# Kernel tuning notes

Hardware: AMD Instinct MI355X
Metric: run time of the kernel (lower is better)

## Reference

```python
import jax, jax.numpy as jnp
import numpy as np

B = 8
D_MODEL = 512
N_HEADS = 8
D_HEAD = 64
D_FF = 2048
N_ENC = 4
N_DEC = 4
SRC_LEN = 512
TGT_LEN = 512
PRED_LEN = 96
SRC_SIZE = 16
TGT_SIZE = 8
EPS = 1e-5
W_SCALE = 0.02


def setup_inputs() -> dict:
    key = jax.random.key(0)
    ks = iter(jax.random.split(key, 64))

    def w(shape):
        return jax.random.normal(next(ks), shape, dtype=jnp.float32) * W_SCALE

    d, f = D_MODEL, D_FF
    inp = {
        "src": jax.random.normal(next(ks), (B, SRC_LEN, SRC_SIZE), dtype=jnp.float32),
        "tgt": jax.random.normal(next(ks), (B, TGT_LEN, TGT_SIZE), dtype=jnp.float32),
        "src_pos_emb": w((SRC_LEN, d)),
        "tgt_pos_emb": w((TGT_LEN, d)),
        "src_lin_w": w((SRC_SIZE, d)), "src_lin_b": jnp.zeros((d,), jnp.float32),
        "tgt_lin_w": w((TGT_SIZE, d)), "tgt_lin_b": jnp.zeros((d,), jnp.float32),
        # encoder stacks [N_ENC, ...]
        "enc_wq": w((N_ENC, d, d)), "enc_wk": w((N_ENC, d, d)),
        "enc_wv": w((N_ENC, d, d)), "enc_wo": w((N_ENC, d, d)),
        "enc_ff1_w": w((N_ENC, d, f)), "enc_ff1_b": jnp.zeros((N_ENC, f), jnp.float32),
        "enc_ff2_w": w((N_ENC, f, d)), "enc_ff2_b": jnp.zeros((N_ENC, d), jnp.float32),
        "enc_ln1_g": jnp.ones((N_ENC, d), jnp.float32), "enc_ln1_b": jnp.zeros((N_ENC, d), jnp.float32),
        "enc_ln2_g": jnp.ones((N_ENC, d), jnp.float32), "enc_ln2_b": jnp.zeros((N_ENC, d), jnp.float32),
        # decoder stacks [N_DEC, ...]
        "dec_sa_wq": w((N_DEC, d, d)), "dec_sa_wk": w((N_DEC, d, d)),
        "dec_sa_wv": w((N_DEC, d, d)), "dec_sa_wo": w((N_DEC, d, d)),
        "dec_ca_wq": w((N_DEC, d, d)), "dec_ca_wk": w((N_DEC, d, d)),
        "dec_ca_wv": w((N_DEC, d, d)), "dec_ca_wo": w((N_DEC, d, d)),
        "dec_ff1_w": w((N_DEC, d, f)), "dec_ff1_b": jnp.zeros((N_DEC, f), jnp.float32),
        "dec_ff2_w": w((N_DEC, f, d)), "dec_ff2_b": jnp.zeros((N_DEC, d), jnp.float32),
        "dec_ln1_g": jnp.ones((N_DEC, d), jnp.float32), "dec_ln1_b": jnp.zeros((N_DEC, d), jnp.float32),
        "dec_ln2_g": jnp.ones((N_DEC, d), jnp.float32), "dec_ln2_b": jnp.zeros((N_DEC, d), jnp.float32),
        "dec_ln3_g": jnp.ones((N_DEC, d), jnp.float32), "dec_ln3_b": jnp.zeros((N_DEC, d), jnp.float32),
        "proj_w": w((d, TGT_SIZE)), "proj_b": jnp.zeros((TGT_SIZE,), jnp.float32),
    }
    return inp


def layer_norm(x, g, b):
    mu = jnp.mean(x, axis=-1, keepdims=True)
    var = jnp.mean(jnp.square(x - mu), axis=-1, keepdims=True)
    return (x - mu) * jax.lax.rsqrt(var + EPS) * g + b


def mha(x_q, x_kv, wq, wk, wv, wo, mask):
    Bq, Lq, _ = x_q.shape
    Lk = x_kv.shape[1]
    q = (x_q @ wq).reshape(Bq, Lq, N_HEADS, D_HEAD)
    k = (x_kv @ wk).reshape(Bq, Lk, N_HEADS, D_HEAD)
    v = (x_kv @ wv).reshape(Bq, Lk, N_HEADS, D_HEAD)
    scores = jnp.einsum("bqhd,bkhd->bhqk", q, k) / jnp.sqrt(
        jnp.asarray(D_HEAD, jnp.float32))
    if mask is not None:
        scores = scores + mask  # broadcast over batch/heads
    attn = jax.nn.softmax(scores, axis=-1)
    ctx = jnp.einsum("bhqk,bkhd->bqhd", attn, v).reshape(Bq, Lq, N_HEADS * D_HEAD)
    return ctx @ wo


def dec_self_mask():
    # get_subsequence_mask with pt=0: -inf on last PRED_LEN key columns
    m = jnp.zeros((TGT_LEN, TGT_LEN), jnp.float32)
    return m.at[:, -PRED_LEN:].set(-jnp.inf)


def reference(src, tgt, src_pos_emb, tgt_pos_emb, src_lin_w, src_lin_b,
              tgt_lin_w, tgt_lin_b,
              enc_wq, enc_wk, enc_wv, enc_wo, enc_ff1_w, enc_ff1_b,
              enc_ff2_w, enc_ff2_b, enc_ln1_g, enc_ln1_b, enc_ln2_g, enc_ln2_b,
              dec_sa_wq, dec_sa_wk, dec_sa_wv, dec_sa_wo,
              dec_ca_wq, dec_ca_wk, dec_ca_wv, dec_ca_wo,
              dec_ff1_w, dec_ff1_b, dec_ff2_w, dec_ff2_b,
              dec_ln1_g, dec_ln1_b, dec_ln2_g, dec_ln2_b, dec_ln3_g, dec_ln3_b,
              proj_w, proj_b):
    # input projections + positional embedding (dropout disabled, eval mode)
    enc_x = src_pos_emb[None] + src @ src_lin_w + src_lin_b
    dec_x = tgt_pos_emb[None] + tgt @ tgt_lin_w + tgt_lin_b

    # encoder (enc_self_attn_mask is None)
    for i in range(N_ENC):
        a = mha(enc_x, enc_x, enc_wq[i], enc_wk[i], enc_wv[i], enc_wo[i], None)
        enc_x = layer_norm(a + enc_x, enc_ln1_g[i], enc_ln1_b[i])
        h = jax.nn.relu(enc_x @ enc_ff1_w[i] + enc_ff1_b[i]) @ enc_ff2_w[i] + enc_ff2_b[i]
        enc_x = layer_norm(h + enc_x, enc_ln2_g[i], enc_ln2_b[i])

    sa_mask = dec_self_mask()  # [tgt_len, tgt_len]
    for i in range(N_DEC):
        a = mha(dec_x, dec_x, dec_sa_wq[i], dec_sa_wk[i], dec_sa_wv[i],
                dec_sa_wo[i], sa_mask)
        dec_x = layer_norm(a + dec_x, dec_ln1_g[i], dec_ln1_b[i])
        a = mha(dec_x, enc_x, dec_ca_wq[i], dec_ca_wk[i], dec_ca_wv[i],
                dec_ca_wo[i], None)
        dec_x = layer_norm(a + dec_x, dec_ln2_g[i], dec_ln2_b[i])
        h = jax.nn.relu(dec_x @ dec_ff1_w[i] + dec_ff1_b[i]) @ dec_ff2_w[i] + dec_ff2_b[i]
        dec_x = layer_norm(h + dec_x, dec_ln3_g[i], dec_ln3_b[i])

    return dec_x @ proj_w + proj_b  # [B, tgt_len, tgt_size]
```

## Files before the change

### kernel.cpp

```cpp
#include <hip/hip_runtime.h>
#include <hip/hip_bf16.h>
#include <math.h>

#define D_MODEL 512
#define N_HEADS 8
#define D_HEAD  64
#define D_FF    2048
#define SEQ     512
#define BATCH   8
#define ROWS    (BATCH * SEQ)
#define PRED_LEN 96
#define KLEN_MASKED (SEQ - PRED_LEN)
#define LN_EPS  1e-5f

typedef float  f32x4 __attribute__((ext_vector_type(4)));
typedef short  s16x8 __attribute__((ext_vector_type(8)));

__device__ __forceinline__ float bf2f(ushort u) {
    union { unsigned int i; float f; } c; c.i = ((unsigned int)u) << 16; return c.f;
}
__device__ __forceinline__ ushort f2bf(float v) {
    __hip_bfloat16 h = __float2bfloat16(v);
    return *(ushort*)&h;
}
__device__ __forceinline__ void gl_lds16(const void* g, void* lds) {
    __builtin_amdgcn_global_load_lds(
        (const __attribute__((address_space(1))) unsigned int*)g,
        (__attribute__((address_space(3))) unsigned int*)lds, 16, 0, 0);
}

__device__ __forceinline__ void swz8(int& x, int& y, int gx, int gy) {
    int n = gx * gy;
    int id = x + gx * y;
    int id2 = (id & 7) * (n >> 3) + (id >> 3);
    x = id2 % gx;
    y = id2 / gx;
}

struct GDesc {
    const ushort* A; int lda;
    const ushort* Bt; int ldb;
    ushort* C; int ldc;
    int N; int K;
    const float* bias; int relu;
    ushort* VT; int vcol0;
};

__device__ __forceinline__ void gemm_body(const GDesc& d, int bx, int by)
{
    __shared__ __attribute__((aligned(16))) ushort As[2][128 * 64];
    __shared__ __attribute__((aligned(16))) ushort Bs[2][64 * 64];
    const int tid = threadIdx.x;
    const int w = tid >> 6, lane = tid & 63;
    const int l16 = lane & 15, quad = lane >> 4;
    const int m0 = by * 128, n0 = bx * 64;
    const ushort* Ab = d.A + (size_t)m0 * d.lda;
    const ushort* Bb = d.Bt + (size_t)n0 * d.ldb;
    const int wm = (w >> 1) * 64, wn = (w & 1) * 32;
    const int nk = d.K >> 6;
    const int lr = lane >> 3, lc = lane & 7;
    const int ch = lc ^ lr;

    auto stage = [&](int buf, int k0) {
        #pragma unroll
        for (int q = 0; q < 4; ++q) {
            int seg = q * 4 + w;
            int row = seg * 8 + lr;
            gl_lds16(Ab + (size_t)row * d.lda + k0 + ch * 8,
                     (void*)(As[buf] + seg * 512));
        }
        #pragma unroll
        for (int q = 0; q < 2; ++q) {
            int seg = q * 4 + w;
            int row = seg * 8 + lr;
            gl_lds16(Bb + (size_t)row * d.ldb + k0 + ch * 8,
                     (void*)(Bs[buf] + seg * 512));
        }
    };

    f32x4 acc[4][2];
    #pragma unroll
    for (int i = 0; i < 4; ++i)
        #pragma unroll
        for (int j = 0; j < 2; ++j) acc[i][j] = (f32x4)0.f;

    auto compute = [&](int buf) {
        #pragma unroll
        for (int t2 = 0; t2 < 2; ++t2) {
            s16x8 af[4];
            #pragma unroll
            for (int i = 0; i < 4; ++i) {
                int r = wm + i * 16 + l16;
                int p = (t2 * 4 + quad) ^ (r & 7);
                af[i] = *(const s16x8*)(As[buf] + r * 64 + p * 8);
            }
            #pragma unroll
            for (int j = 0; j < 2; ++j) {
                int r = wn + j * 16 + l16;
                int p = (t2 * 4 + quad) ^ (r & 7);
                s16x8 bfr = *(const s16x8*)(Bs[buf] + r * 64 + p * 8);
                #pragma unroll
                for (int i = 0; i < 4; ++i)
                    acc[i][j] = __builtin_amdgcn_mfma_f32_16x16x32_bf16(af[i], bfr, acc[i][j], 0, 0, 0);
            }
        }
    };

    stage(0, 0);
    __syncthreads();
    int cur = 0;
    for (int t = 0; t < nk - 1; ++t) {
        stage(cur ^ 1, (t + 1) << 6);
        compute(cur);
        __syncthreads();
        cur ^= 1;
    }
    compute(cur);

    const bool isv = (d.VT != nullptr) && (n0 >= d.vcol0);
    if (isv) {
        #pragma unroll
        for (int i = 0; i < 4; ++i) {
            int mrow = m0 + wm + i * 16 + quad * 4;
            int b = mrow >> 9, pbase = mrow & 511;
            #pragma unroll
            for (int j = 0; j < 2; ++j) {
                int cv = n0 + wn + j * 16 + l16 - d.vcol0;
                int h = cv >> 6, dd = cv & 63;
                union { ushort u[4]; uint2 v; } pk;
                #pragma unroll
                for (int r = 0; r < 4; ++r) pk.u[r] = f2bf(acc[i][j][r]);
                *(uint2*)(d.VT + ((size_t)((b * 8 + h) * 64 + dd) * 512 + pbase)) = pk.v;
            }
        }
    } else {
        #pragma unroll
        for (int i = 0; i < 4; ++i) {
            #pragma unroll
            for (int j = 0; j < 2; ++j) {
                int col = n0 + wn + j * 16 + l16;
                float bv = d.bias ? d.bias[col] : 0.f;
                #pragma unroll
                for (int r = 0; r < 4; ++r) {
                    float v = acc[i][j][r] + bv;
                    if (d.relu) v = fmaxf(v, 0.f);
                    d.C[(size_t)(m0 + wm + i * 16 + quad * 4 + r) * d.ldc + col] = f2bf(v);
                }
            }
        }
    }
}

__global__ __launch_bounds__(256) void gemm_one(GDesc d)
{
    int bx = blockIdx.x, by = blockIdx.y;
    swz8(bx, by, gridDim.x, gridDim.y);
    if (bx * 64 < d.N) gemm_body(d, bx, by);
}

__global__ __launch_bounds__(256) void gemm_two(GDesc d0, GDesc d1)
{
    const GDesc& d = blockIdx.z ? d1 : d0;
    int bx = blockIdx.x, by = blockIdx.y;
    swz8(bx, by, gridDim.x, gridDim.y);
    if (bx * 64 < d.N) gemm_body(d, bx, by);
}

struct SKDesc {
    const ushort* A; int lda;
    const ushort* Bt; int ldb;
    float* P;
    int K;
};

__global__ __launch_bounds__(256) void gemm_sk(SKDesc d)
{
    __shared__ __attribute__((aligned(16))) ushort As[2][128 * 64];
    __shared__ __attribute__((aligned(16))) ushort Bs[2][64 * 64];
    const int tid = threadIdx.x;
    const int w = tid >> 6, lane = tid & 63;
    const int l16 = lane & 15, quad = lane >> 4;
    int bx = blockIdx.x, by = blockIdx.y;
    swz8(bx, by, gridDim.x, gridDim.y);
    const int m0 = by * 128, n0 = bx * 64;
    const int slice = blockIdx.z;
    const int kb = slice * (d.K >> 1);
    const int nk = d.K >> 7;
    const ushort* Ab = d.A + (size_t)m0 * d.lda + kb;
    const ushort* Bb = d.Bt + (size_t)n0 * d.ldb + kb;
    const int wm = (w >> 1) * 64, wn = (w & 1) * 32;
    const int lr = lane >> 3, lc = lane & 7;
    const int ch = lc ^ lr;

    auto stage = [&](int buf, int k0) {
        #pragma unroll
        for (int q = 0; q < 4; ++q) {
            int seg = q * 4 + w;
            int row = seg * 8 + lr;
            gl_lds16(Ab + (size_t)row * d.lda + k0 + ch * 8,
                     (void*)(As[buf] + seg * 512));
        }
        #pragma unroll
        for (int q = 0; q < 2; ++q) {
            int seg = q * 4 + w;
            int row = seg * 8 + lr;
            gl_lds16(Bb + (size_t)row * d.ldb + k0 + ch * 8,
                     (void*)(Bs[buf] + seg * 512));
        }
    };

    f32x4 acc[4][2];
    #pragma unroll
    for (int i = 0; i < 4; ++i)
        #pragma unroll
        for (int j = 0; j < 2; ++j) acc[i][j] = (f32x4)0.f;

    auto compute = [&](int buf) {
        #pragma unroll
        for (int t2 = 0; t2 < 2; ++t2) {
            s16x8 af[4];
            #pragma unroll
            for (int i = 0; i < 4; ++i) {
                int r = wm + i * 16 + l16;
                int p = (t2 * 4 + quad) ^ (r & 7);
                af[i] = *(const s16x8*)(As[buf] + r * 64 + p * 8);
            }
            #pragma unroll
            for (int j = 0; j < 2; ++j) {
                int r = wn + j * 16 + l16;
                int p = (t2 * 4 + quad) ^ (r & 7);
                s16x8 bfr = *(const s16x8*)(Bs[buf] + r * 64 + p * 8);
                #pragma unroll
                for (int i = 0; i < 4; ++i)
                    acc[i][j] = __builtin_amdgcn_mfma_f32_16x16x32_bf16(af[i], bfr, acc[i][j], 0, 0, 0);
            }
        }
    };

    stage(0, 0);
    __syncthreads();
    int cur = 0;
    for (int t = 0; t < nk - 1; ++t) {
        stage(cur ^ 1, (t + 1) << 6);
        compute(cur);
        __syncthreads();
        cur ^= 1;
    }
    compute(cur);

    float* P = d.P + (size_t)slice * ((size_t)ROWS * 512);
    #pragma unroll
    for (int i = 0; i < 4; ++i) {
        #pragma unroll
        for (int j = 0; j < 2; ++j) {
            int col = n0 + wn + j * 16 + l16;
            #pragma unroll
            for (int r = 0; r < 4; ++r)
                P[(size_t)(m0 + wm + i * 16 + quad * 4 + r) * 512 + col] = acc[i][j][r];
        }
    }
}

__global__ __launch_bounds__(256) void flash_attn(
    const ushort* __restrict__ Q, int ldq,
    const ushort* __restrict__ K, int ldk,
    const ushort* __restrict__ Vt,
    ushort* __restrict__ O, int ldo, int klen)
{
    __shared__ __attribute__((aligned(16))) ushort KVs[8192];
    __shared__ __attribute__((aligned(16))) ushort Es[4][2048];
    const int tid = threadIdx.x, w = tid >> 6, lane = tid & 63;
    const int l16 = lane & 15, quad = lane >> 4;
    int bqx = blockIdx.x, bhy = blockIdx.y;
    swz8(bqx, bhy, gridDim.x, gridDim.y);
    const int bh = bhy, b = bh >> 3, h = bh & 7;
    const int q0 = bqx * 64;

    const ushort* Qb = Q + (size_t)(b * SEQ) * ldq + h * D_HEAD;
    const ushort* Kb = K + (size_t)(b * SEQ) * ldk + h * D_HEAD;
    const ushort* Vb = Vt + (size_t)bh * (D_HEAD * SEQ);

    auto stageK = [&](int kc) {
        #pragma unroll
        for (int it = 0; it < 4; ++it) {
            int cc = (it * 4 + w) * 64 + lane;
            int row = cc >> 3;
            int dch = (cc & 7) ^ (row & 7);
            gl_lds16(Kb + (size_t)(kc * 128 + row) * ldk + dch * 8,
                     (void*)(KVs + (size_t)(it * 4 + w) * 512));
        }
    };
    auto stageV = [&](int kc) {
        #pragma unroll
        for (int it = 0; it < 4; ++it) {
            int cc = (it * 4 + w) * 64 + lane;
            int dd = cc >> 4;
            int kch = (cc & 15) ^ (dd & 15);
            gl_lds16(Vb + (size_t)dd * SEQ + kc * 128 + kch * 8,
                     (void*)(KVs + (size_t)(it * 4 + w) * 512));
        }
    };

    stageK(0);

    s16x8 af0, af1;
    {
        const ushort* qr = Qb + (size_t)(q0 + w * 16 + l16) * ldq + quad * 8;
        af0 = *(const s16x8*)(qr);
        af1 = *(const s16x8*)(qr + 32);
    }

    f32x4 sc[32];

    #pragma unroll
    for (int kc = 0; kc < 4; ++kc) {
        if (kc > 0) stageK(kc);
        __syncthreads();
        #pragma unroll
        for (int kt = 0; kt < 8; ++kt) {
            int r0 = kt * 16 + l16;
            s16x8 b0 = *(const s16x8*)(KVs + r0 * 64 + ((quad)     ^ (r0 & 7)) * 8);
            s16x8 b1 = *(const s16x8*)(KVs + r0 * 64 + ((4 + quad) ^ (r0 & 7)) * 8);
            f32x4 a = __builtin_amdgcn_mfma_f32_16x16x32_bf16(af0, b0, (f32x4)0.f, 0, 0, 0);
            sc[kc * 8 + kt] = __builtin_amdgcn_mfma_f32_16x16x32_bf16(af1, b1, a, 0, 0, 0);
        }
        __syncthreads();
    }

    stageV(0);

    float inv[4];
    #pragma unroll
    for (int r = 0; r < 4; ++r) {
        float m = -1e30f;
        #pragma unroll
        for (int j = 0; j < 32; ++j) {
            bool valid = (j * 16 + l16) < klen;
            m = valid ? fmaxf(m, sc[j][r]) : m;
        }
        m = fmaxf(m, __shfl_xor(m, 1));
        m = fmaxf(m, __shfl_xor(m, 2));
        m = fmaxf(m, __shfl_xor(m, 4));
        m = fmaxf(m, __shfl_xor(m, 8));
        float ssum = 0.f;
        #pragma unroll
        for (int j = 0; j < 32; ++j) {
            bool valid = (j * 16 + l16) < klen;
            float e = valid ? __expf((sc[j][r] - m) * 0.125f) : 0.f;
            sc[j][r] = e;
            ssum += e;
        }
        ssum += __shfl_xor(ssum, 1);
        ssum += __shfl_xor(ssum, 2);
        ssum += __shfl_xor(ssum, 4);
        ssum += __shfl_xor(ssum, 8);
        inv[r] = 1.f / ssum;
    }

    f32x4 oacc[4];
    #pragma unroll
    for (int jd = 0; jd < 4; ++jd) oacc[jd] = (f32x4)0.f;
    #pragma unroll
    for (int kc = 0; kc < 4; ++kc) {
        if (kc > 0) stageV(kc);
        #pragma unroll
        for (int j = 0; j < 8; ++j) {
            int lcj = j * 2 + (l16 >> 3);
            #pragma unroll
            for (int r = 0; r < 4; ++r) {
                int m = quad * 4 + r;
                Es[w][m * 128 + (lcj ^ m) * 8 + (l16 & 7)] = f2bf(sc[kc * 8 + j][r]);
            }
        }
        __syncthreads();
        #pragma unroll
        for (int ks = 0; ks < 4; ++ks) {
            int lc = ks * 4 + quad;
            s16x8 ea = *(const s16x8*)(&Es[w][l16 * 128 + (lc ^ l16) * 8]);
            #pragma unroll
            for (int jd = 0; jd < 4; ++jd) {
                int row = jd * 16 + l16;
                s16x8 vb = *(const s16x8*)(KVs + row * 128 + (lc ^ l16) * 8);
                oacc[jd] = __builtin_amdgcn_mfma_f32_16x16x32_bf16(ea, vb, oacc[jd], 0, 0, 0);
            }
        }
        __syncthreads();
    }

    ushort* Ob = O + (size_t)(b * SEQ) * ldo + h * D_HEAD;
    #pragma unroll
    for (int jd = 0; jd < 4; ++jd)
        #pragma unroll
        for (int r = 0; r < 4; ++r)
            Ob[(size_t)(q0 + w * 16 + quad * 4 + r) * ldo + jd * 16 + l16] =
                f2bf(oacc[jd][r] * inv[r]);
}

struct AttnPtrs { const float* p[48]; };
struct FfPtrs   { const float* p[16]; };

__global__ __launch_bounds__(256) void repack_attn(AttnPtrs L, ushort* __restrict__ out)
{
    int z = blockIdx.z;
    const float* in = L.p[z];
    ushort* o = out + (size_t)z * 262144;
    __shared__ float t[32][33];
    int n0 = blockIdx.x * 32, k0 = blockIdx.y * 32;
    int tx = threadIdx.x & 31, ty = threadIdx.x >> 5;
    #pragma unroll
    for (int r = 0; r < 4; ++r)
        t[ty + r * 8][tx] = in[(size_t)(k0 + ty + r * 8) * 512 + n0 + tx];
    __syncthreads();
    #pragma unroll
    for (int r = 0; r < 4; ++r)
        o[(size_t)(n0 + ty + r * 8) * 512 + k0 + tx] = f2bf(t[tx][ty + r * 8]);
}

__global__ __launch_bounds__(256) void repack_ff(FfPtrs L, ushort* __restrict__ out)
{
    int z = blockIdx.y;
    int Kd = (z < 8) ? 512 : 2048, Nd = (z < 8) ? 2048 : 512;
    const float* in = L.p[z];
    ushort* o = out + (size_t)z * (512 * 2048);
    int t = blockIdx.x;
    int tn = Nd / 32;
    int n0 = (t % tn) * 32, k0 = (t / tn) * 32;
    __shared__ float ts[32][33];
    int tx = threadIdx.x & 31, ty = threadIdx.x >> 5;
    #pragma unroll
    for (int r = 0; r < 4; ++r)
        ts[ty + r * 8][tx] = in[(size_t)(k0 + ty + r * 8) * Nd + n0 + tx];
    __syncthreads();
    #pragma unroll
    for (int r = 0; r < 4; ++r)
        o[(size_t)(n0 + ty + r * 8) * Kd + k0 + tx] = f2bf(ts[tx][ty + r * 8]);
}

__global__ __launch_bounds__(256) void input_proj2(
    const float* __restrict__ x0, const float* __restrict__ w0,
    const float* __restrict__ b0, const float* __restrict__ p0,
    float* __restrict__ o0_32, ushort* __restrict__ o0_b, int in0,
    const float* __restrict__ x1, const float* __restrict__ w1,
    const float* __restrict__ b1, const float* __restrict__ p1,
    float* __restrict__ o1_32, ushort* __restrict__ o1_b, int in1)
{
    const int z = blockIdx.y;
    const float* x = z ? x1 : x0;  const float* w = z ? w1 : w0;
    const float* bias = z ? b1 : b0; const float* pos = z ? p1 : p0;
    float* out32 = z ? o1_32 : o0_32; ushort* outb = z ? o1_b : o0_b;
    int in_size = z ? in1 : in0;
    int idx = blockIdx.x * 256 + threadIdx.x;
    int col = idx & (D_MODEL - 1);
    int row = idx >> 9;
    int l   = row & (SEQ - 1);
    const float* xr = x + (size_t)row * in_size;
    float acc = bias[col] + pos[(size_t)l * D_MODEL + col];
    for (int t = 0; t < in_size; ++t) acc += xr[t] * w[(size_t)t * D_MODEL + col];
    out32[idx] = acc;
    outb[idx]  = f2bf(acc);
}

__global__ __launch_bounds__(256) void add_ln2(
    const float* __restrict__ p, const float* __restrict__ gb,
    const float* __restrict__ x,
    const float* __restrict__ g, const float* __restrict__ b,
    float* __restrict__ out32, ushort* __restrict__ outb)
{
    const int row  = blockIdx.x * 4 + (threadIdx.x >> 6);
    const int lane = threadIdx.x & 63;
    const int c0   = lane * 8;
    const size_t base = (size_t)row * D_MODEL + c0;
    const float* p1 = p + (size_t)ROWS * 512;
    f32x4 a0 = *(const f32x4*)(p + base),  a1 = *(const f32x4*)(p + base + 4);
    f32x4 c0v= *(const f32x4*)(p1 + base), c1v= *(const f32x4*)(p1 + base + 4);
    f32x4 x0 = *(const f32x4*)(x + base),  x1 = *(const f32x4*)(x + base + 4);
    float v[8];
    #pragma unroll
    for (int j = 0; j < 4; ++j) {
        v[j]     = a0[j] + c0v[j] + x0[j];
        v[4 + j] = a1[j] + c1v[j] + x1[j];
    }
    if (gb) {
        f32x4 gb0 = *(const f32x4*)(gb + c0), gb1 = *(const f32x4*)(gb + c0 + 4);
        #pragma unroll
        for (int j = 0; j < 4; ++j) { v[j] += gb0[j]; v[4 + j] += gb1[j]; }
    }
    float s = 0.f;
    #pragma unroll
    for (int j = 0; j < 8; ++j) s += v[j];
    #pragma unroll
    for (int off = 32; off; off >>= 1) s += __shfl_xor(s, off);
    float mu = s * (1.f / D_MODEL);
    float q = 0.f;
    #pragma unroll
    for (int j = 0; j < 8; ++j) { v[j] -= mu; q += v[j] * v[j]; }
    #pragma unroll
    for (int off = 32; off; off >>= 1) q += __shfl_xor(q, off);
    float rs = rsqrtf(q * (1.f / D_MODEL) + LN_EPS);
    f32x4 g0 = *(const f32x4*)(g + c0), g1 = *(const f32x4*)(g + c0 + 4);
    f32x4 b0 = *(const f32x4*)(b + c0), b1 = *(const f32x4*)(b + c0 + 4);
    f32x4 y0, y1;
    union { ushort u[8]; s16x8 w; } pk;
    #pragma unroll
    for (int j = 0; j < 4; ++j) {
        y0[j] = v[j]     * rs * g0[j] + b0[j];
        y1[j] = v[4 + j] * rs * g1[j] + b1[j];
        pk.u[j]     = f2bf(y0[j]);
        pk.u[4 + j] = f2bf(y1[j]);
    }
    *(f32x4*)(out32 + base)     = y0;
    *(f32x4*)(out32 + base + 4) = y1;
    *(s16x8*)(outb + base)      = pk.w;
}

__global__ __launch_bounds__(256) void final_proj(
    const float* __restrict__ X, const float* __restrict__ W,
    const float* __restrict__ b, float* __restrict__ out)
{
    const int row  = blockIdx.x * 4 + (threadIdx.x >> 6);
    const int lane = threadIdx.x & 63;
    const float* xr = X + (size_t)row * D_MODEL + lane * 8;
    f32x4 x0 = *(const f32x4*)(xr), x1 = *(const f32x4*)(xr + 4);
    const float* wr = W + (size_t)lane * 64;
    f32x4 pa = (f32x4)0.f, pb = (f32x4)0.f;
    #pragma unroll
    for (int j = 0; j < 8; ++j) {
        float xv = (j < 4) ? x0[j] : x1[j - 4];
        f32x4 w0 = *(const f32x4*)(wr + j * 8);
        f32x4 w1 = *(const f32x4*)(wr + j * 8 + 4);
        #pragma unroll
        for (int c = 0; c < 4; ++c) { pa[c] += xv * w0[c]; pb[c] += xv * w1[c]; }
    }
    #pragma unroll
    for (int off = 32; off; off >>= 1) {
        #pragma unroll
        for (int c = 0; c < 4; ++c) {
            pa[c] += __shfl_xor(pa[c], off);
            pb[c] += __shfl_xor(pb[c], off);
        }
    }
    if (lane == 0) {
        float* o = out + (size_t)row * 8;
        #pragma unroll
        for (int c = 0; c < 4; ++c) { o[c] = pa[c] + b[c]; o[4 + c] = pb[c] + b[4 + c]; }
    }
}

extern "C" void kernel_launch(void* const* d_in, const int* in_sizes, int n_in,
                              void* d_out, int out_size, void* d_ws, size_t ws_size,
                              hipStream_t stream)
{
    const float* src         = (const float*)d_in[0];
    const float* tgt         = (const float*)d_in[1];
    const float* src_pos     = (const float*)d_in[2];
    const float* tgt_pos     = (const float*)d_in[3];
    const float* src_lin_w   = (const float*)d_in[4];
    const float* src_lin_b   = (const float*)d_in[5];
    const float* tgt_lin_w   = (const float*)d_in[6];
    const float* tgt_lin_b   = (const float*)d_in[7];
    const float* enc_wq      = (const float*)d_in[8];
    const float* enc_wk      = (const float*)d_in[9];
    const float* enc_wv      = (const float*)d_in[10];
    const float* enc_wo      = (const float*)d_in[11];
    const float* enc_ff1_w   = (const float*)d_in[12];
    const float* enc_ff1_b   = (const float*)d_in[13];
    const float* enc_ff2_w   = (const float*)d_in[14];
    const float* enc_ff2_b   = (const float*)d_in[15];
    const float* enc_ln1_g   = (const float*)d_in[16];
    const float* enc_ln1_b   = (const float*)d_in[17];
    const float* enc_ln2_g   = (const float*)d_in[18];
    const float* enc_ln2_b   = (const float*)d_in[19];
    const float* dec_sa_wq   = (const float*)d_in[20];
    const float* dec_sa_wk   = (const float*)d_in[21];
    const float* dec_sa_wv   = (const float*)d_in[22];
    const float* dec_sa_wo   = (const float*)d_in[23];
    const float* dec_ca_wq   = (const float*)d_in[24];
    const float* dec_ca_wk   = (const float*)d_in[25];
    const float* dec_ca_wv   = (const float*)d_in[26];
    const float* dec_ca_wo   = (const float*)d_in[27];
    const float* dec_ff1_w   = (const float*)d_in[28];
    const float* dec_ff1_b   = (const float*)d_in[29];
    const float* dec_ff2_w   = (const float*)d_in[30];
    const float* dec_ff2_b   = (const float*)d_in[31];
    const float* dec_ln1_g   = (const float*)d_in[32];
    const float* dec_ln1_b   = (const float*)d_in[33];
    const float* dec_ln2_g   = (const float*)d_in[34];
    const float* dec_ln2_b   = (const float*)d_in[35];
    const float* dec_ln3_g   = (const float*)d_in[36];
    const float* dec_ln3_b   = (const float*)d_in[37];
    const float* proj_w      = (const float*)d_in[38];
    const float* proj_b      = (const float*)d_in[39];

    char* p = (char*)d_ws;
    auto carve = [&](size_t bytes) { char* r = p; p += (bytes + 255) & ~(size_t)255; return r; };
    ushort* enc_xb = (ushort*)carve((size_t)ROWS * D_MODEL * 2);
    ushort* dec_xb = (ushort*)carve((size_t)ROWS * D_MODEL * 2);
    float*  enc_x32= (float*) carve((size_t)ROWS * D_MODEL * 4);
    float*  dec_x32= (float*) carve((size_t)ROWS * D_MODEL * 4);
    ushort* qkvb   = (ushort*)carve((size_t)ROWS * 1536 * 2);
    ushort* qb     = (ushort*)carve((size_t)ROWS * D_MODEL * 2);
    ushort* kvb    = (ushort*)carve((size_t)ROWS * 1024 * 2);
    ushort* ctxb   = (ushort*)carve((size_t)ROWS * D_MODEL * 2);
    float*  pf     = (float*) carve((size_t)2 * ROWS * D_MODEL * 4);
    ushort* ffhb   = (ushort*)carve((size_t)ROWS * D_FF * 2);
    ushort* vt     = (ushort*)carve((size_t)64 * D_HEAD * SEQ * 2);
    ushort* wa     = (ushort*)carve((size_t)48 * 262144 * 2);
    ushort* wf     = (ushort*)carve((size_t)16 * 1048576 * 2);

    const dim3 blk(256);

    {
        AttnPtrs A;
        for (int i = 0; i < 4; ++i) {
            const size_t o = (size_t)i * 262144;
            A.p[i * 3 + 0] = enc_wq + o;  A.p[i * 3 + 1] = enc_wk + o;  A.p[i * 3 + 2] = enc_wv + o;
            A.p[12 + i] = enc_wo + o;
            A.p[16 + i * 3 + 0] = dec_sa_wq + o; A.p[16 + i * 3 + 1] = dec_sa_wk + o;
            A.p[16 + i * 3 + 2] = dec_sa_wv + o;
            A.p[28 + i] = dec_sa_wo + o;
            A.p[32 + i * 2 + 0] = dec_ca_wk + o; A.p[32 + i * 2 + 1] = dec_ca_wv + o;
            A.p[40 + i] = dec_ca_wq + o;
            A.p[44 + i] = dec_ca_wo + o;
        }
        repack_attn<<<dim3(16, 16, 48), blk, 0, stream>>>(A, wa);
        FfPtrs F;
        for (int i = 0; i < 4; ++i) {
            F.p[0 + i]  = enc_ff1_w + (size_t)i * 1048576;
            F.p[4 + i]  = dec_ff1_w + (size_t)i * 1048576;
            F.p[8 + i]  = enc_ff2_w + (size_t)i * 1048576;
            F.p[12 + i] = dec_ff2_w + (size_t)i * 1048576;
        }
        repack_ff<<<dim3(1024, 16), blk, 0, stream>>>(F, wf);
    }

    auto mkd = [&](const ushort* A, int lda, const ushort* Bt, int ldb,
                   ushort* C, int ldc, int N, int K,
                   const float* bias, int relu, ushort* VT, int vcol0) {
        GDesc d; d.A = A; d.lda = lda; d.Bt = Bt; d.ldb = ldb;
        d.C = C; d.ldc = ldc; d.N = N; d.K = K;
        d.bias = bias; d.relu = relu; d.VT = VT; d.vcol0 = vcol0;
        return d;
    };
    auto g64 = [&](const GDesc& d) {
        gemm_one<<<dim3(d.N / 64, ROWS / 128), blk, 0, stream>>>(d);
    };
    auto gsk = [&](const ushort* A, int lda, const ushort* Bt, int K) {
        SKDesc d; d.A = A; d.lda = lda; d.Bt = Bt; d.ldb = K; d.P = pf; d.K = K;
        gemm_sk<<<dim3(8, ROWS / 128, 2), blk, 0, stream>>>(d);
    };

    input_proj2<<<dim3(ROWS * D_MODEL / 256, 2), blk, 0, stream>>>(
        src, src_lin_w, src_lin_b, src_pos, enc_x32, enc_xb, 16,
        tgt, tgt_lin_w, tgt_lin_b, tgt_pos, dec_x32, dec_xb, 8);

    for (int i = 0; i < 4; ++i) {
        g64(mkd(enc_xb, 512, wa + (size_t)(i * 3) * 262144, 512, qkvb, 1536,
                1536, 512, nullptr, 0, vt, 1024));
        flash_attn<<<dim3(8, 64), blk, 0, stream>>>(qkvb, 1536, qkvb + 512, 1536, vt,
                                                    ctxb, D_MODEL, SEQ);
        gsk(ctxb, 512, wa + (size_t)(12 + i) * 262144, 512);
        add_ln2<<<ROWS / 4, blk, 0, stream>>>(pf, nullptr, enc_x32,
                                              enc_ln1_g + i * 512, enc_ln1_b + i * 512,
                                              enc_x32, enc_xb);
        g64(mkd(enc_xb, 512, wf + (size_t)i * 1048576, 512, ffhb, 2048,
                2048, 512, enc_ff1_b + i * 2048, 1, nullptr, 0));
        gsk(ffhb, 2048, wf + (size_t)(8 + i) * 1048576, 2048);
        add_ln2<<<ROWS / 4, blk, 0, stream>>>(pf, enc_ff2_b + i * 512, enc_x32,
                                              enc_ln2_g + i * 512, enc_ln2_b + i * 512,
                                              enc_x32, enc_xb);
    }

    for (int i = 0; i < 4; ++i) {
        g64(mkd(dec_xb, 512, wa + (size_t)(16 + i * 3) * 262144, 512, qkvb, 1536,
                1536, 512, nullptr, 0, vt, 1024));
        flash_attn<<<dim3(8, 64), blk, 0, stream>>>(qkvb, 1536, qkvb + 512, 1536, vt,
                                                    ctxb, D_MODEL, KLEN_MASKED);
        gsk(ctxb, 512, wa + (size_t)(28 + i) * 262144, 512);
        add_ln2<<<ROWS / 4, blk, 0, stream>>>(pf, nullptr, dec_x32,
                                              dec_ln1_g + i * 512, dec_ln1_b + i * 512,
                                              dec_x32, dec_xb);
        {
            GDesc dq = mkd(dec_xb, 512, wa + (size_t)(40 + i) * 262144, 512, qb, 512,
                           512, 512, nullptr, 0, nullptr, 0);
            GDesc dkv = mkd(enc_xb, 512, wa + (size_t)(32 + i * 2) * 262144, 512, kvb, 1024,
                            1024, 512, nullptr, 0, vt, 512);
            gemm_two<<<dim3(16, ROWS / 128, 2), blk, 0, stream>>>(dq, dkv);
        }
        flash_attn<<<dim3(8, 64), blk, 0, stream>>>(qb, 512, kvb, 1024, vt,
                                                    ctxb, D_MODEL, SEQ);
        gsk(ctxb, 512, wa + (size_t)(44 + i) * 262144, 512);
        add_ln2<<<ROWS / 4, blk, 0, stream>>>(pf, nullptr, dec_x32,
                                              dec_ln2_g + i * 512, dec_ln2_b + i * 512,
                                              dec_x32, dec_xb);
        g64(mkd(dec_xb, 512, wf + (size_t)(4 + i) * 1048576, 512, ffhb, 2048,
                2048, 512, dec_ff1_b + i * 2048, 1, nullptr, 0));
        gsk(ffhb, 2048, wf + (size_t)(12 + i) * 1048576, 2048);
        add_ln2<<<ROWS / 4, blk, 0, stream>>>(pf, dec_ff2_b + i * 512, dec_x32,
                                              dec_ln3_g + i * 512, dec_ln3_b + i * 512,
                                              dec_x32, dec_xb);
    }

    final_proj<<<ROWS / 4, blk, 0, stream>>>(dec_x32, proj_w, proj_b, (float*)d_out);
}
```

Before: 1.228 ms.

## Batch encoder and decoder layer-0 self-attention blocks into shared launches

The decoder's first self-attention block does not depend on the encoder, so its QKV GEMM, flash attention, output-projection split-K GEMM and add+LayerNorm are now launched together with the encoder's layer-0 equivalents. Each pair runs as one kernel selected by grid z or y. This halves the launch count for those stages and fills the GPU with twice as many blocks. It needs duplicate scratch buffers (qkvb2, vt2, ctxb2, pf2) and adds a descriptor select in each kernel.

Result: no change. 1.248 ms (+1.6%).

```diff
diff --git a/kernel.cpp b/kernel.cpp
--- a/kernel.cpp
+++ b/kernel.cpp
@@ -173,7 +173,7 @@
     int K;
 };
 
-__global__ __launch_bounds__(256) void gemm_sk(SKDesc d)
+__device__ __forceinline__ void sk_body(const SKDesc& d, int slice)
 {
     __shared__ __attribute__((aligned(16))) ushort As[2][128 * 64];
     __shared__ __attribute__((aligned(16))) ushort Bs[2][64 * 64];
@@ -183,7 +183,6 @@
     int bx = blockIdx.x, by = blockIdx.y;
     swz8(bx, by, gridDim.x, gridDim.y);
     const int m0 = by * 128, n0 = bx * 64;
-    const int slice = blockIdx.z;
     const int kb = slice * (d.K >> 1);
     const int nk = d.K >> 7;
     const ushort* Ab = d.A + (size_t)m0 * d.lda + kb;
@@ -261,11 +260,24 @@
     }
 }
 
-__global__ __launch_bounds__(256) void flash_attn(
-    const ushort* __restrict__ Q, int ldq,
-    const ushort* __restrict__ K, int ldk,
-    const ushort* __restrict__ Vt,
-    ushort* __restrict__ O, int ldo, int klen)
+__global__ __launch_bounds__(256) void gemm_sk(SKDesc d)
+{
+    sk_body(d, blockIdx.z);
+}
+
+__global__ __launch_bounds__(256) void gemm_sk2(SKDesc d0, SKDesc d1)
+{
+    sk_body((blockIdx.z >> 1) ? d1 : d0, blockIdx.z & 1);
+}
+
+struct FA {
+    const ushort* Q; int ldq;
+    const ushort* K; int ldk;
+    const ushort* Vt;
+    ushort* O; int ldo; int klen;
+};
+
+__device__ __forceinline__ void flash_body(const FA& f)
 {
     __shared__ __attribute__((aligned(16))) ushort KVs[8192];
     __shared__ __attribute__((aligned(16))) ushort Es[4][2048];
@@ -276,9 +288,9 @@
     const int bh = bhy, b = bh >> 3, h = bh & 7;
     const int q0 = bqx * 64;
 
-    const ushort* Qb = Q + (size_t)(b * SEQ) * ldq + h * D_HEAD;
-    const ushort* Kb = K + (size_t)(b * SEQ) * ldk + h * D_HEAD;
-    const ushort* Vb = Vt + (size_t)bh * (D_HEAD * SEQ);
+    const ushort* Qb = f.Q + (size_t)(b * SEQ) * f.ldq + h * D_HEAD;
+    const ushort* Kb = f.K + (size_t)(b * SEQ) * f.ldk + h * D_HEAD;
+    const ushort* Vb = f.Vt + (size_t)bh * (D_HEAD * SEQ);
 
     auto stageK = [&](int kc) {
         #pragma unroll
@@ -286,7 +298,7 @@
             int cc = (it * 4 + w) * 64 + lane;
             int row = cc >> 3;
             int dch = (cc & 7) ^ (row & 7);
-            gl_lds16(Kb + (size_t)(kc * 128 + row) * ldk + dch * 8,
+            gl_lds16(Kb + (size_t)(kc * 128 + row) * f.ldk + dch * 8,
                      (void*)(KVs + (size_t)(it * 4 + w) * 512));
         }
     };
@@ -305,7 +317,7 @@
 
     s16x8 af0, af1;
     {
-        const ushort* qr = Qb + (size_t)(q0 + w * 16 + l16) * ldq + quad * 8;
+        const ushort* qr = Qb + (size_t)(q0 + w * 16 + l16) * f.ldq + quad * 8;
         af0 = *(const s16x8*)(qr);
         af1 = *(const s16x8*)(qr + 32);
     }
@@ -335,7 +347,7 @@
         float m = -1e30f;
         #pragma unroll
         for (int j = 0; j < 32; ++j) {
-            bool valid = (j * 16 + l16) < klen;
+            bool valid = (j * 16 + l16) < f.klen;
             m = valid ? fmaxf(m, sc[j][r]) : m;
         }
         m = fmaxf(m, __shfl_xor(m, 1));
@@ -345,7 +357,7 @@
         float ssum = 0.f;
         #pragma unroll
         for (int j = 0; j < 32; ++j) {
-            bool valid = (j * 16 + l16) < klen;
+            bool valid = (j * 16 + l16) < f.klen;
             float e = valid ? __expf((sc[j][r] - m) * 0.125f) : 0.f;
             sc[j][r] = e;
             ssum += e;
@@ -387,13 +399,20 @@
         __syncthreads();
     }
 
-    ushort* Ob = O + (size_t)(b * SEQ) * ldo + h * D_HEAD;
+    ushort* Ob = f.O + (size_t)(b * SEQ) * f.ldo + h * D_HEAD;
     #pragma unroll
     for (int jd = 0; jd < 4; ++jd)
         #pragma unroll
         for (int r = 0; r < 4; ++r)
-            Ob[(size_t)(q0 + w * 16 + quad * 4 + r) * ldo + jd * 16 + l16] =
+            Ob[(size_t)(q0 + w * 16 + quad * 4 + r) * f.ldo + jd * 16 + l16] =
                 f2bf(oacc[jd][r] * inv[r]);
+}
+
+__global__ __launch_bounds__(256) void flash_one(FA f) { flash_body(f); }
+
+__global__ __launch_bounds__(256) void flash_two(FA f0, FA f1)
+{
+    flash_body(blockIdx.z ? f1 : f0);
 }
 
 struct AttnPtrs { const float* p[48]; };
@@ -460,28 +479,31 @@
     outb[idx]  = f2bf(acc);
 }
 
-__global__ __launch_bounds__(256) void add_ln2(
-    const float* __restrict__ p, const float* __restrict__ gb,
-    const float* __restrict__ x,
-    const float* __restrict__ g, const float* __restrict__ b,
-    float* __restrict__ out32, ushort* __restrict__ outb)
+struct LN {
+    const float* p; const float* gb;
+    const float* x;
+    const float* g; const float* b;
+    float* out32; ushort* outb;
+};
+
+__device__ __forceinline__ void ln_body(const LN& d)
 {
     const int row  = blockIdx.x * 4 + (threadIdx.x >> 6);
     const int lane = threadIdx.x & 63;
     const int c0   = lane * 8;
     const size_t base = (size_t)row * D_MODEL + c0;
-    const float* p1 = p + (size_t)ROWS * 512;
-    f32x4 a0 = *(const f32x4*)(p + base),  a1 = *(const f32x4*)(p + base + 4);
-    f32x4 c0v= *(const f32x4*)(p1 + base), c1v= *(const f32x4*)(p1 + base + 4);
-    f32x4 x0 = *(const f32x4*)(x + base),  x1 = *(const f32x4*)(x + base + 4);
+    const float* p1 = d.p + (size_t)ROWS * 512;
+    f32x4 a0 = *(const f32x4*)(d.p + base),  a1 = *(const f32x4*)(d.p + base + 4);
+    f32x4 c0v= *(const f32x4*)(p1 + base),   c1v= *(const f32x4*)(p1 + base + 4);
+    f32x4 x0 = *(const f32x4*)(d.x + base),  x1 = *(const f32x4*)(d.x + base + 4);
     float v[8];
     #pragma unroll
     for (int j = 0; j < 4; ++j) {
         v[j]     = a0[j] + c0v[j] + x0[j];
         v[4 + j] = a1[j] + c1v[j] + x1[j];
     }
-    if (gb) {
-        f32x4 gb0 = *(const f32x4*)(gb + c0), gb1 = *(const f32x4*)(gb + c0 + 4);
+    if (d.gb) {
+        f32x4 gb0 = *(const f32x4*)(d.gb + c0), gb1 = *(const f32x4*)(d.gb + c0 + 4);
         #pragma unroll
         for (int j = 0; j < 4; ++j) { v[j] += gb0[j]; v[4 + j] += gb1[j]; }
     }
@@ -497,8 +519,8 @@
     #pragma unroll
     for (int off = 32; off; off >>= 1) q += __shfl_xor(q, off);
     float rs = rsqrtf(q * (1.f / D_MODEL) + LN_EPS);
-    f32x4 g0 = *(const f32x4*)(g + c0), g1 = *(const f32x4*)(g + c0 + 4);
-    f32x4 b0 = *(const f32x4*)(b + c0), b1 = *(const f32x4*)(b + c0 + 4);
+    f32x4 g0 = *(const f32x4*)(d.g + c0), g1 = *(const f32x4*)(d.g + c0 + 4);
+    f32x4 b0 = *(const f32x4*)(d.b + c0), b1 = *(const f32x4*)(d.b + c0 + 4);
     f32x4 y0, y1;
     union { ushort u[8]; s16x8 w; } pk;
     #pragma unroll
@@ -508,9 +530,16 @@
         pk.u[j]     = f2bf(y0[j]);
         pk.u[4 + j] = f2bf(y1[j]);
     }
-    *(f32x4*)(out32 + base)     = y0;
-    *(f32x4*)(out32 + base + 4) = y1;
-    *(s16x8*)(outb + base)      = pk.w;
+    *(f32x4*)(d.out32 + base)     = y0;
+    *(f32x4*)(d.out32 + base + 4) = y1;
+    *(s16x8*)(d.outb + base)      = pk.w;
+}
+
+__global__ __launch_bounds__(256) void add_ln_one(LN d) { ln_body(d); }
+
+__global__ __launch_bounds__(256) void add_ln_two(LN d0, LN d1)
+{
+    ln_body(blockIdx.y ? d1 : d0);
 }
 
 __global__ __launch_bounds__(256) void final_proj(
@@ -598,12 +627,16 @@
     float*  enc_x32= (float*) carve((size_t)ROWS * D_MODEL * 4);
     float*  dec_x32= (float*) carve((size_t)ROWS * D_MODEL * 4);
     ushort* qkvb   = (ushort*)carve((size_t)ROWS * 1536 * 2);
+    ushort* qkvb2  = (ushort*)carve((size_t)ROWS * 1536 * 2);
     ushort* qb     = (ushort*)carve((size_t)ROWS * D_MODEL * 2);
     ushort* kvb    = (ushort*)carve((size_t)ROWS * 1024 * 2);
     ushort* ctxb   = (ushort*)carve((size_t)ROWS * D_MODEL * 2);
+    ushort* ctxb2  = (ushort*)carve((size_t)ROWS * D_MODEL * 2);
     float*  pf     = (float*) carve((size_t)2 * ROWS * D_MODEL * 4);
+    float*  pf2    = (float*) carve((size_t)2 * ROWS * D_MODEL * 4);
     ushort* ffhb   = (ushort*)carve((size_t)ROWS * D_FF * 2);
     ushort* vt     = (ushort*)carve((size_t)64 * D_HEAD * SEQ * 2);
+    ushort* vt2    = (ushort*)carve((size_t)64 * D_HEAD * SEQ * 2);
     ushort* wa     = (ushort*)carve((size_t)48 * 262144 * 2);
     ushort* wf     = (ushort*)carve((size_t)16 * 1048576 * 2);
 
@@ -641,44 +674,81 @@
         d.bias = bias; d.relu = relu; d.VT = VT; d.vcol0 = vcol0;
         return d;
     };
+    auto mksk = [&](const ushort* A, int lda, const ushort* Bt, int K, float* P) {
+        SKDesc d; d.A = A; d.lda = lda; d.Bt = Bt; d.ldb = K; d.P = P; d.K = K;
+        return d;
+    };
+    auto mkfa = [&](const ushort* Q, int ldq, const ushort* K, int ldk,
+                    const ushort* Vt, ushort* O, int klen) {
+        FA f; f.Q = Q; f.ldq = ldq; f.K = K; f.ldk = ldk; f.Vt = Vt;
+        f.O = O; f.ldo = D_MODEL; f.klen = klen;
+        return f;
+    };
+    auto mkln = [&](const float* pp, const float* gb, float* x32,
+                    const float* g, const float* b, ushort* outb) {
+        LN d; d.p = pp; d.gb = gb; d.x = x32; d.g = g; d.b = b;
+        d.out32 = x32; d.outb = outb;
+        return d;
+    };
     auto g64 = [&](const GDesc& d) {
         gemm_one<<<dim3(d.N / 64, ROWS / 128), blk, 0, stream>>>(d);
-    };
-    auto gsk = [&](const ushort* A, int lda, const ushort* Bt, int K) {
-        SKDesc d; d.A = A; d.lda = lda; d.Bt = Bt; d.ldb = K; d.P = pf; d.K = K;
-        gemm_sk<<<dim3(8, ROWS / 128, 2), blk, 0, stream>>>(d);
     };
 
     input_proj2<<<dim3(ROWS * D_MODEL / 256, 2), blk, 0, stream>>>(
         src, src_lin_w, src_lin_b, src_pos, enc_x32, enc_xb, 16,
         tgt, tgt_lin_w, tgt_lin_b, tgt_pos, dec_x32, dec_xb, 8);
 
+    {
+        GDesc qe = mkd(enc_xb, 512, wa, 512, qkvb, 1536, 1536, 512,
+                       nullptr, 0, vt, 1024);
+        GDesc qd = mkd(dec_xb, 512, wa + (size_t)16 * 262144, 512, qkvb2, 1536,
+                       1536, 512, nullptr, 0, vt2, 1024);
+        gemm_two<<<dim3(24, ROWS / 128, 2), blk, 0, stream>>>(qe, qd);
+
+        FA fe = mkfa(qkvb, 1536, qkvb + 512, 1536, vt, ctxb, SEQ);
+        FA fd = mkfa(qkvb2, 1536, qkvb2 + 512, 1536, vt2, ctxb2, KLEN_MASKED);
+        flash_two<<<dim3(8, 64, 2), blk, 0, stream>>>(fe, fd);
+
+        SKDesc se = mksk(ctxb, 512, wa + (size_t)12 * 262144, 512, pf);
+        SKDesc sd = mksk(ctxb2, 512, wa + (size_t)28 * 262144, 512, pf2);
+        gemm_sk2<<<dim3(8, ROWS / 128, 4), blk, 0, stream>>>(se, sd);
+
+        LN le = mkln(pf, nullptr, enc_x32, enc_ln1_g, enc_ln1_b, enc_xb);
+        LN ld = mkln(pf2, nullptr, dec_x32, dec_ln1_g, dec_ln1_b, dec_xb);
+        add_ln_two<<<dim3(ROWS / 4, 2), blk, 0, stream>>>(le, ld);
+    }
+
     for (int i = 0; i < 4; ++i) {
-        g64(mkd(enc_xb, 512, wa + (size_t)(i * 3) * 262144, 512, qkvb, 1536,
-                1536, 512, nullptr, 0, vt, 1024));
-        flash_attn<<<dim3(8, 64), blk, 0, stream>>>(qkvb, 1536, qkvb + 512, 1536, vt,
-                                                    ctxb, D_MODEL, SEQ);
-        gsk(ctxb, 512, wa + (size_t)(12 + i) * 262144, 512);
-        add_ln2<<<ROWS / 4, blk, 0, stream>>>(pf, nullptr, enc_x32,
-                                              enc_ln1_g + i * 512, enc_ln1_b + i * 512,
-                                              enc_x32, enc_xb);
+        if (i > 0) {
+            g64(mkd(enc_xb, 512, wa + (size_t)(i * 3) * 262144, 512, qkvb, 1536,
+                    1536, 512, nullptr, 0, vt, 1024));
+            flash_one<<<dim3(8, 64), blk, 0, stream>>>(
+                mkfa(qkvb, 1536, qkvb + 512, 1536, vt, ctxb, SEQ));
+            gemm_sk<<<dim3(8, ROWS / 128, 2), blk, 0, stream>>>(
+                mksk(ctxb, 512, wa + (size_t)(12 + i) * 262144, 512, pf));
+            add_ln_one<<<ROWS / 4, blk, 0, stream>>>(
+                mkln(pf, nullptr, enc_x32, enc_ln1_g + i * 512, enc_ln1_b + i * 512, enc_xb));
+        }
         g64(mkd(enc_xb, 512, wf + (size_t)i * 1048576, 512, ffhb, 2048,
                 2048, 512, enc_ff1_b + i * 2048, 1, nullptr, 0));
-        gsk(ffhb, 2048, wf + (size_t)(8 + i) * 1048576, 2048);
-        add_ln2<<<ROWS / 4, blk, 0, stream>>>(pf, enc_ff2_b + i * 512, enc_x32,
-                                              enc_ln2_g + i * 512, enc_ln2_b + i * 512,
-                                              enc_x32, enc_xb);
+        gemm_sk<<<dim3(8, ROWS / 128, 2), blk, 0, stream>>>(
+            mksk(ffhb, 2048, wf + (size_t)(8 + i) * 1048576, 2048, pf));
+        add_ln_one<<<ROWS / 4, blk, 0, stream>>>(
+            mkln(pf, enc_ff2_b + i * 512, enc_x32,
+                 enc_ln2_g + i * 512, enc_ln2_b + i * 512, enc_xb));
     }
 
     for (int i = 0; i < 4; ++i) {
-        g64(mkd(dec_xb, 512, wa + (size_t)(16 + i * 3) * 262144, 512, qkvb, 1536,
-                1536, 512, nullptr, 0, vt, 1024));
-        flash_attn<<<dim3(8, 64), blk, 0, stream>>>(qkvb, 1536, qkvb + 512, 1536, vt,
-                                                    ctxb, D_MODEL, KLEN_MASKED);
-        gsk(ctxb, 512, wa + (size_t)(28 + i) * 262144, 512);
-        add_ln2<<<ROWS / 4, blk, 0, stream>>>(pf, nullptr, dec_x32,
-                                              dec_ln1_g + i * 512, dec_ln1_b + i * 512,
-                                              dec_x32, dec_xb);
+        if (i > 0) {
+            g64(mkd(dec_xb, 512, wa + (size_t)(16 + i * 3) * 262144, 512, qkvb, 1536,
+                    1536, 512, nullptr, 0, vt, 1024));
+            flash_one<<<dim3(8, 64), blk, 0, stream>>>(
+                mkfa(qkvb, 1536, qkvb + 512, 1536, vt, ctxb, KLEN_MASKED));
+            gemm_sk<<<dim3(8, ROWS / 128, 2), blk, 0, stream>>>(
+                mksk(ctxb, 512, wa + (size_t)(28 + i) * 262144, 512, pf));
+            add_ln_one<<<ROWS / 4, blk, 0, stream>>>(
+                mkln(pf, nullptr, dec_x32, dec_ln1_g + i * 512, dec_ln1_b + i * 512, dec_xb));
+        }
         {
             GDesc dq = mkd(dec_xb, 512, wa + (size_t)(40 + i) * 262144, 512, qb, 512,
                            512, 512, nullptr, 0, nullptr, 0);
@@ -686,18 +756,19 @@
                             1024, 512, nullptr, 0, vt, 512);
             gemm_two<<<dim3(16, ROWS / 128, 2), blk, 0, stream>>>(dq, dkv);
         }
-        flash_attn<<<dim3(8, 64), blk, 0, stream>>>(qb, 512, kvb, 1024, vt,
-                                                    ctxb, D_MODEL, SEQ);
-        gsk(ctxb, 512, wa + (size_t)(44 + i) * 262144, 512);
-        add_ln2<<<ROWS / 4, blk, 0, stream>>>(pf, nullptr, dec_x32,
-                                              dec_ln2_g + i * 512, dec_ln2_b + i * 512,
-                                              dec_x32, dec_xb);
+        flash_one<<<dim3(8, 64), blk, 0, stream>>>(
+            mkfa(qb, 512, kvb, 1024, vt, ctxb, SEQ));
+        gemm_sk<<<dim3(8, ROWS / 128, 2), blk, 0, stream>>>(
+            mksk(ctxb, 512, wa + (size_t)(44 + i) * 262144, 512, pf));
+        add_ln_one<<<ROWS / 4, blk, 0, stream>>>(
+            mkln(pf, nullptr, dec_x32, dec_ln2_g + i * 512, dec_ln2_b + i * 512, dec_xb));
         g64(mkd(dec_xb, 512, wf + (size_t)(4 + i) * 1048576, 512, ffhb, 2048,
                 2048, 512, dec_ff1_b + i * 2048, 1, nullptr, 0));
-        gsk(ffhb, 2048, wf + (size_t)(12 + i) * 1048576, 2048);
-        add_ln2<<<ROWS / 4, blk, 0, stream>>>(pf, dec_ff2_b + i * 512, dec_x32,
-                                              dec_ln3_g + i * 512, dec_ln3_b + i * 512,
-                                              dec_x32, dec_xb);
+        gemm_sk<<<dim3(8, ROWS / 128, 2), blk, 0, stream>>>(
+            mksk(ffhb, 2048, wf + (size_t)(12 + i) * 1048576, 2048, pf));
+        add_ln_one<<<ROWS / 4, blk, 0, stream>>>(
+            mkln(pf, dec_ff2_b + i * 512, dec_x32,
+                 dec_ln3_g + i * 512, dec_ln3_b + i * 512, dec_xb));
     }
 
     final_proj<<<ROWS / 4, blk, 0, stream>>>(dec_x32, proj_w, proj_b, (float*)d_out);
```

## Halve flash-attention tile to 32 query rows, skip masked key tiles, merge repacks

Applied to the files above, without the earlier changes.

Flash attention now runs with two waves per block covering 32 query rows instead of four waves covering 64, which doubles the grid to 1024 blocks so more workgroups can be resident across CUs. K/V staging loops double their iterations so the smaller block still fills the shared tile. QK^T MFMAs are skipped for key tiles lying wholly beyond klen, cutting work in the masked decoder self-attention. The two weight repack kernels are merged into one launch. The cost is that each block re-stages K/V for half as many queries, doubling K/V loads from global memory.

Result: faster. 1.165 ms (-5.1%).

```diff
diff --git a/kernel.cpp b/kernel.cpp
--- a/kernel.cpp
+++ b/kernel.cpp
@@ -261,20 +261,20 @@
     }
 }
 
-__global__ __launch_bounds__(256) void flash_attn(
+__global__ __launch_bounds__(128) void flash_attn(
     const ushort* __restrict__ Q, int ldq,
     const ushort* __restrict__ K, int ldk,
     const ushort* __restrict__ Vt,
     ushort* __restrict__ O, int ldo, int klen)
 {
     __shared__ __attribute__((aligned(16))) ushort KVs[8192];
-    __shared__ __attribute__((aligned(16))) ushort Es[4][2048];
+    __shared__ __attribute__((aligned(16))) ushort Es[2][2048];
     const int tid = threadIdx.x, w = tid >> 6, lane = tid & 63;
     const int l16 = lane & 15, quad = lane >> 4;
     int bqx = blockIdx.x, bhy = blockIdx.y;
     swz8(bqx, bhy, gridDim.x, gridDim.y);
     const int bh = bhy, b = bh >> 3, h = bh & 7;
-    const int q0 = bqx * 64;
+    const int q0 = bqx * 32;
 
     const ushort* Qb = Q + (size_t)(b * SEQ) * ldq + h * D_HEAD;
     const ushort* Kb = K + (size_t)(b * SEQ) * ldk + h * D_HEAD;
@@ -282,22 +282,22 @@
 
     auto stageK = [&](int kc) {
         #pragma unroll
-        for (int it = 0; it < 4; ++it) {
-            int cc = (it * 4 + w) * 64 + lane;
+        for (int it = 0; it < 8; ++it) {
+            int cc = (it * 2 + w) * 64 + lane;
             int row = cc >> 3;
             int dch = (cc & 7) ^ (row & 7);
             gl_lds16(Kb + (size_t)(kc * 128 + row) * ldk + dch * 8,
-                     (void*)(KVs + (size_t)(it * 4 + w) * 512));
+                     (void*)(KVs + (size_t)(it * 2 + w) * 512));
         }
     };
     auto stageV = [&](int kc) {
         #pragma unroll
-        for (int it = 0; it < 4; ++it) {
-            int cc = (it * 4 + w) * 64 + lane;
+        for (int it = 0; it < 8; ++it) {
+            int cc = (it * 2 + w) * 64 + lane;
             int dd = cc >> 4;
             int kch = (cc & 15) ^ (dd & 15);
             gl_lds16(Vb + (size_t)dd * SEQ + kc * 128 + kch * 8,
-                     (void*)(KVs + (size_t)(it * 4 + w) * 512));
+                     (void*)(KVs + (size_t)(it * 2 + w) * 512));
         }
     };
 
@@ -318,11 +318,13 @@
         __syncthreads();
         #pragma unroll
         for (int kt = 0; kt < 8; ++kt) {
-            int r0 = kt * 16 + l16;
-            s16x8 b0 = *(const s16x8*)(KVs + r0 * 64 + ((quad)     ^ (r0 & 7)) * 8);
-            s16x8 b1 = *(const s16x8*)(KVs + r0 * 64 + ((4 + quad) ^ (r0 & 7)) * 8);
-            f32x4 a = __builtin_amdgcn_mfma_f32_16x16x32_bf16(af0, b0, (f32x4)0.f, 0, 0, 0);
-            sc[kc * 8 + kt] = __builtin_amdgcn_mfma_f32_16x16x32_bf16(af1, b1, a, 0, 0, 0);
+            if (kc * 128 + kt * 16 < klen) {
+                int r0 = kt * 16 + l16;
+                s16x8 b0 = *(const s16x8*)(KVs + r0 * 64 + ((quad)     ^ (r0 & 7)) * 8);
+                s16x8 b1 = *(const s16x8*)(KVs + r0 * 64 + ((4 + quad) ^ (r0 & 7)) * 8);
+                f32x4 a = __builtin_amdgcn_mfma_f32_16x16x32_bf16(af0, b0, (f32x4)0.f, 0, 0, 0);
+                sc[kc * 8 + kt] = __builtin_amdgcn_mfma_f32_16x16x32_bf16(af1, b1, a, 0, 0, 0);
+            }
         }
         __syncthreads();
     }
@@ -399,41 +401,40 @@
 struct AttnPtrs { const float* p[48]; };
 struct FfPtrs   { const float* p[16]; };
 
-__global__ __launch_bounds__(256) void repack_attn(AttnPtrs L, ushort* __restrict__ out)
-{
-    int z = blockIdx.z;
-    const float* in = L.p[z];
-    ushort* o = out + (size_t)z * 262144;
+__global__ __launch_bounds__(256) void repack_all(
+    AttnPtrs A, FfPtrs F, ushort* __restrict__ wa, ushort* __restrict__ wf)
+{
     __shared__ float t[32][33];
-    int n0 = blockIdx.x * 32, k0 = blockIdx.y * 32;
-    int tx = threadIdx.x & 31, ty = threadIdx.x >> 5;
-    #pragma unroll
-    for (int r = 0; r < 4; ++r)
-        t[ty + r * 8][tx] = in[(size_t)(k0 + ty + r * 8) * 512 + n0 + tx];
-    __syncthreads();
-    #pragma unroll
-    for (int r = 0; r < 4; ++r)
-        o[(size_t)(n0 + ty + r * 8) * 512 + k0 + tx] = f2bf(t[tx][ty + r * 8]);
-}
-
-__global__ __launch_bounds__(256) void repack_ff(FfPtrs L, ushort* __restrict__ out)
-{
-    int z = blockIdx.y;
-    int Kd = (z < 8) ? 512 : 2048, Nd = (z < 8) ? 2048 : 512;
-    const float* in = L.p[z];
-    ushort* o = out + (size_t)z * (512 * 2048);
-    int t = blockIdx.x;
-    int tn = Nd / 32;
-    int n0 = (t % tn) * 32, k0 = (t / tn) * 32;
-    __shared__ float ts[32][33];
-    int tx = threadIdx.x & 31, ty = threadIdx.x >> 5;
-    #pragma unroll
-    for (int r = 0; r < 4; ++r)
-        ts[ty + r * 8][tx] = in[(size_t)(k0 + ty + r * 8) * Nd + n0 + tx];
-    __syncthreads();
-    #pragma unroll
-    for (int r = 0; r < 4; ++r)
-        o[(size_t)(n0 + ty + r * 8) * Kd + k0 + tx] = f2bf(ts[tx][ty + r * 8]);
+    const int tx = threadIdx.x & 31, ty = threadIdx.x >> 5;
+    const int id = blockIdx.x;
+    if (id < 12288) {
+        int z = id >> 8, tt = id & 255;
+        int n0 = (tt & 15) * 32, k0 = (tt >> 4) * 32;
+        const float* in = A.p[z];
+        ushort* o = wa + (size_t)z * 262144;
+        #pragma unroll
+        for (int r = 0; r < 4; ++r)
+            t[ty + r * 8][tx] = in[(size_t)(k0 + ty + r * 8) * 512 + n0 + tx];
+        __syncthreads();
+        #pragma unroll
+        for (int r = 0; r < 4; ++r)
+            o[(size_t)(n0 + ty + r * 8) * 512 + k0 + tx] = f2bf(t[tx][ty + r * 8]);
+    } else {
+        int id2 = id - 12288;
+        int z = id2 >> 10, tt = id2 & 1023;
+        int Kd = (z < 8) ? 512 : 2048, Nd = (z < 8) ? 2048 : 512;
+        const float* in = F.p[z];
+        ushort* o = wf + (size_t)z * (512 * 2048);
+        int tn = Nd / 32;
+        int n0 = (tt % tn) * 32, k0 = (tt / tn) * 32;
+        #pragma unroll
+        for (int r = 0; r < 4; ++r)
+            t[ty + r * 8][tx] = in[(size_t)(k0 + ty + r * 8) * Nd + n0 + tx];
+        __syncthreads();
+        #pragma unroll
+        for (int r = 0; r < 4; ++r)
+            o[(size_t)(n0 + ty + r * 8) * Kd + k0 + tx] = f2bf(t[tx][ty + r * 8]);
+    }
 }
 
 __global__ __launch_bounds__(256) void input_proj2(
@@ -622,7 +623,6 @@
             A.p[40 + i] = dec_ca_wq + o;
             A.p[44 + i] = dec_ca_wo + o;
         }
-        repack_attn<<<dim3(16, 16, 48), blk, 0, stream>>>(A, wa);
         FfPtrs F;
         for (int i = 0; i < 4; ++i) {
             F.p[0 + i]  = enc_ff1_w + (size_t)i * 1048576;
@@ -630,7 +630,7 @@
             F.p[8 + i]  = enc_ff2_w + (size_t)i * 1048576;
             F.p[12 + i] = dec_ff2_w + (size_t)i * 1048576;
         }
-        repack_ff<<<dim3(1024, 16), blk, 0, stream>>>(F, wf);
+        repack_all<<<dim3(12288 + 16384), blk, 0, stream>>>(A, F, wa, wf);
     }
 
     auto mkd = [&](const ushort* A, int lda, const ushort* Bt, int ldb,
@@ -656,8 +656,8 @@
     for (int i = 0; i < 4; ++i) {
         g64(mkd(enc_xb, 512, wa + (size_t)(i * 3) * 262144, 512, qkvb, 1536,
                 1536, 512, nullptr, 0, vt, 1024));
-        flash_attn<<<dim3(8, 64), blk, 0, stream>>>(qkvb, 1536, qkvb + 512, 1536, vt,
-                                                    ctxb, D_MODEL, SEQ);
+        flash_attn<<<dim3(16, 64), dim3(128), 0, stream>>>(qkvb, 1536, qkvb + 512, 1536, vt,
+                                                           ctxb, D_MODEL, SEQ);
         gsk(ctxb, 512, wa + (size_t)(12 + i) * 262144, 512);
         add_ln2<<<ROWS / 4, blk, 0, stream>>>(pf, nullptr, enc_x32,
                                               enc_ln1_g + i * 512, enc_ln1_b + i * 512,
@@ -673,8 +673,8 @@
     for (int i = 0; i < 4; ++i) {
         g64(mkd(dec_xb, 512, wa + (size_t)(16 + i * 3) * 262144, 512, qkvb, 1536,
                 1536, 512, nullptr, 0, vt, 1024));
-        flash_attn<<<dim3(8, 64), blk, 0, stream>>>(qkvb, 1536, qkvb + 512, 1536, vt,
-                                                    ctxb, D_MODEL, KLEN_MASKED);
+        flash_attn<<<dim3(16, 64), dim3(128), 0, stream>>>(qkvb, 1536, qkvb + 512, 1536, vt,
+                                                           ctxb, D_MODEL, KLEN_MASKED);
         gsk(ctxb, 512, wa + (size_t)(28 + i) * 262144, 512);
         add_ln2<<<ROWS / 4, blk, 0, stream>>>(pf, nullptr, dec_x32,
                                               dec_ln1_g + i * 512, dec_ln1_b + i * 512,
@@ -686,8 +686,8 @@
                             1024, 512, nullptr, 0, vt, 512);
             gemm_two<<<dim3(16, ROWS / 128, 2), blk, 0, stream>>>(dq, dkv);
         }
-        flash_attn<<<dim3(8, 64), blk, 0, stream>>>(qb, 512, kvb, 1024, vt,
-                                                    ctxb, D_MODEL, SEQ);
+        flash_attn<<<dim3(16, 64), dim3(128), 0, stream>>>(qb, 512, kvb, 1024, vt,
+                                                           ctxb, D_MODEL, SEQ);
         gsk(ctxb, 512, wa + (size_t)(44 + i) * 262144, 512);
         add_ln2<<<ROWS / 4, blk, 0, stream>>>(pf, nullptr, dec_x32,
                                               dec_ln2_g + i * 512, dec_ln2_b + i * 512,
```
